# Kernel optimization log

Measured on AMD Instinct MI355X. Metric: run time of the kernel, lower is better.

## Reference

```python
import jax, jax.numpy as jnp
import numpy as np

B, DV, W, H = 64, 2048, 14, 14
DQ, DA, G, DH, NC = 2400, 1200, 2, 1200, 3000


def setup_inputs() -> dict:
    key = jax.random.key(0)
    ks = jax.random.split(key, 14)
    s = lambda k, shp, scale=0.02: jax.random.normal(k, shp, dtype=jnp.float32) * scale
    return {
        "input_q": jax.random.normal(ks[0], (B, DQ), dtype=jnp.float32),
        "input_v": jax.random.normal(ks[1], (B, DV, W, H), dtype=jnp.float32),
        "Wv_att": s(ks[2], (DA, DV)),
        "bv_att": s(ks[3], (DA,)),
        "Wq_att": s(ks[4], (DA, DQ)),
        "bq_att": s(ks[5], (DA,)),
        "Watt": s(ks[6], (G, DA)),
        "batt": s(ks[7], (G,)),
        "Wv_fus": s(ks[8], (G, DH, DV)),
        "bv_fus": s(ks[9], (G, DH)),
        "Wq_fus": s(ks[10], (G * DH, DQ)),
        "bq_fus": s(ks[11], (G * DH,)),
        "Wc": s(ks[12], (NC, G * DH)),
        "bc": s(ks[13], (NC,)),
    }


def reference(input_q, input_v, Wv_att, bv_att, Wq_att, bq_att, Watt, batt,
              Wv_fus, bv_fus, Wq_fus, bq_fus, Wc, bc):
    b, dv, w, h = input_v.shape
    n = w * h  # spatial positions

    # --- attention branch (eval mode: dropout = identity) ---
    # 1x1 conv == per-position linear over channels; activation_v = tanh
    xv = jnp.tanh(jnp.einsum('bchw,dc->bdhw', input_v, Wv_att) + bv_att[None, :, None, None])
    xv = xv.reshape(b, -1, n).transpose(0, 2, 1)               # [B, WH, DA]
    # question projection; activation_q = tanh
    xq = jnp.tanh(input_q @ Wq_att.T + bq_att)                 # [B, DA]
    # MLB Hadamard fusion + activation_mm = tanh
    xatt = jnp.tanh(xv * xq[:, None, :])                       # [B, WH, DA]
    # glimpse scores: 1x1 conv over dim_mm channels
    wgt = jnp.einsum('bnd,gd->bgn', xatt, Watt) + batt[None, :, None]  # [B, G, WH]
    att = jax.nn.softmax(wgt, axis=-1)                         # softmax over WH per glimpse

    # weighted sum of ORIGINAL features per glimpse
    v_flat = input_v.reshape(b, dv, n)                         # [B, DV, WH]
    v_att = jnp.einsum('bgn,bdn->bgd', att, v_flat)            # [B, G, DV]

    # --- glimpse fusion + classification ---
    v_fus = jnp.tanh(jnp.einsum('bgd,ghd->bgh', v_att, Wv_fus) + bv_fus)  # [B, G, DH]
    v_fus = v_fus.reshape(b, -1)                               # [B, G*DH] (concat over glimpses)
    q_fus = jnp.tanh(input_q @ Wq_fus.T + bq_fus)              # [B, G*DH]
    x = (v_fus * q_fus) @ Wc.T + bc                            # [B, NC]
    return (x, wgt)
```

## Files before the change

kernel.cpp:

```cpp
#include <hip/hip_runtime.h>
#include <hip/hip_fp16.h>

typedef _Float16 half8 __attribute__((ext_vector_type(8)));
typedef float f32x4 __attribute__((ext_vector_type(4)));

__device__ __forceinline__ float tanh_fast(float x) {
  float e = __expf(2.0f * x);
  return 1.0f - 2.0f / (e + 1.0f);
}

__device__ __forceinline__ void gload16(const _Float16* g, _Float16* l) {
  __builtin_amdgcn_global_load_lds((const __attribute__((address_space(1))) void*)g,
                                   (__attribute__((address_space(3))) void*)l,
                                   16, 0, 0);
}

__global__ __launch_bounds__(256) void k_transpose_v(const float* __restrict__ in,
                                                     _Float16* __restrict__ out) {
  __shared__ float t[64][65];
  int b = blockIdx.z;
  int c0 = blockIdx.y * 64;
  int p0 = blockIdx.x * 64;
  int tid = threadIdx.x;
  int pl = tid & 63;
  #pragma unroll
  for (int s = 0; s < 16; ++s) {
    int cl = (tid >> 6) + s * 4;
    int p = p0 + pl;
    t[cl][pl] = (p < 196) ? in[((size_t)b * 2048 + (c0 + cl)) * 196 + p] : 0.0f;
  }
  __syncthreads();
  int c8 = (tid & 7) * 8;
  #pragma unroll
  for (int s = 0; s < 2; ++s) {
    int p = p0 + (tid >> 3) + s * 32;
    if (p < 196) {
      half8 v;
      #pragma unroll
      for (int j = 0; j < 8; ++j) v[j] = (_Float16)t[c8 + j][(tid >> 3) + s * 32];
      *(half8*)(out + ((size_t)b * 196 + p) * 2048 + c0 + c8) = v;
    }
  }
}

__global__ __launch_bounds__(256) void k_prep(const float* __restrict__ W,
                                              _Float16* __restrict__ Wh,
                                              const float* __restrict__ batt,
                                              float* __restrict__ wgt) {
  int i = blockIdx.x * 256 + threadIdx.x;
  int n = i >> 11;
  Wh[i] = (n < 1200) ? (_Float16)W[i] : (_Float16)0.0f;
  if (i < 25088) wgt[i] = batt[(i / 196) & 1];
}

__global__ __launch_bounds__(512, 2) void k_gemm1(const _Float16* __restrict__ A,
                                                  const _Float16* __restrict__ B,
                                                  const float* __restrict__ bias,
                                                  const float* __restrict__ xq,
                                                  const float* __restrict__ Watt,
                                                  float* __restrict__ wgt) {
  __shared__ __align__(16) _Float16 AS[2][256 * 64];
  __shared__ __align__(16) _Float16 BS[2][256 * 64];
  int tid = threadIdx.x;
  int n0 = blockIdx.x * 256;
  int m0 = blockIdx.y * 256;
  int lane = tid & 63;
  int wave = tid >> 6;
  int wm = (wave >> 2) * 128;
  int wn = (wave & 3) * 64;
  int fr = lane & 15;
  int fq = lane >> 4;

  int lr = lane >> 3;
  int swz8 = ((lane & 7) ^ lr) << 3;
  const _Float16* aSrc[2][2];
  const _Float16* bSrc[2][2];
  int aDst[2][2], bDst[2][2];
  #pragma unroll
  for (int h = 0; h < 2; ++h)
    #pragma unroll
    for (int j = 0; j < 2; ++j) {
      int ra = j * 128 + h * 64 + wave * 8;
      aSrc[h][j] = A + (size_t)(m0 + ra + lr) * 2048 + swz8;
      aDst[h][j] = ra * 64;
      int rb = (j * 2 + (wave >> 2)) * 64 + h * 32 + (wave & 3) * 8;
      bSrc[h][j] = B + (size_t)(n0 + rb + lr) * 2048 + swz8;
      bDst[h][j] = rb * 64;
    }

  f32x4 acc[8][4];
  #pragma unroll
  for (int i = 0; i < 8; ++i)
    #pragma unroll
    for (int j = 0; j < 4; ++j) acc[i][j] = (f32x4){0.f, 0.f, 0.f, 0.f};

  auto stA = [&](int buf, int h, int k0) {
    gload16(aSrc[h][0] + k0, &AS[buf][aDst[h][0]]);
    gload16(aSrc[h][1] + k0, &AS[buf][aDst[h][1]]);
  };
  auto stB = [&](int buf, int h, int k0) {
    gload16(bSrc[h][0] + k0, &BS[buf][bDst[h][0]]);
    gload16(bSrc[h][1] + k0, &BS[buf][bDst[h][1]]);
  };
  auto dsA = [&](int buf, int mh, half8 (&a)[4][2]) {
    #pragma unroll
    for (int mt = 0; mt < 4; ++mt)
      #pragma unroll
      for (int kk = 0; kk < 2; ++kk) {
        int row = wm + mh * 64 + mt * 16 + fr;
        int c = kk * 4 + fq;
        a[mt][kk] = *(const half8*)(&AS[buf][row * 64 + ((c ^ (row & 7)) << 3)]);
      }
  };
  auto dsB = [&](int buf, int nh, half8 (&b)[2][2]) {
    #pragma unroll
    for (int nt = 0; nt < 2; ++nt)
      #pragma unroll
      for (int kk = 0; kk < 2; ++kk) {
        int row = wn + nh * 32 + nt * 16 + fr;
        int c = kk * 4 + fq;
        b[nt][kk] = *(const half8*)(&BS[buf][row * 64 + ((c ^ (row & 7)) << 3)]);
      }
  };
  auto mma = [&](half8 (&a)[4][2], half8 (&b)[2][2], int mh, int nh) {
    __builtin_amdgcn_s_setprio(1);
    #pragma unroll
    for (int mt = 0; mt < 4; ++mt)
      #pragma unroll
      for (int nt = 0; nt < 2; ++nt)
        #pragma unroll
        for (int kk = 0; kk < 2; ++kk)
          acc[mh * 4 + mt][nh * 2 + nt] = __builtin_amdgcn_mfma_f32_16x16x32_f16(
              a[mt][kk], b[nt][kk], acc[mh * 4 + mt][nh * 2 + nt], 0, 0, 0);
    __builtin_amdgcn_s_setprio(0);
  };

#define BAR() __builtin_amdgcn_s_barrier()
#define LGKM0() do { asm volatile("s_waitcnt lgkmcnt(0)" ::: "memory"); \
                     __builtin_amdgcn_sched_barrier(0); } while (0)

  stA(0, 0, 0); stB(0, 0, 0); stB(0, 1, 0); stA(0, 1, 0);
  stA(1, 0, 64); stB(1, 0, 64); stB(1, 1, 64);
  asm volatile("s_waitcnt vmcnt(6)" ::: "memory");
  BAR();

  half8 a[4][2], b0[2][2], b1[2][2];
  for (int i = 0; i < 16; ++i) {
    const bool nl = (i < 15);
    const int kT = i * 128;
    dsA(0, 0, a); dsB(0, 0, b0);
    stA(1, 1, kT + 64);
    BAR(); LGKM0();
    mma(a, b0, 0, 0);
    BAR();
    dsB(0, 1, b1);
    if (nl) stA(0, 0, kT + 128);
    BAR(); LGKM0();
    mma(a, b1, 0, 1);
    BAR();
    dsA(0, 1, a);
    if (nl) stB(0, 0, kT + 128);
    BAR(); LGKM0();
    mma(a, b1, 1, 1);
    BAR();
    if (nl) {
      stB(0, 1, kT + 128);
      asm volatile("s_waitcnt vmcnt(6)" ::: "memory");
    } else {
      asm volatile("s_waitcnt vmcnt(0)" ::: "memory");
    }
    BAR();
    mma(a, b0, 1, 0);
    BAR();
    dsA(1, 0, a); dsB(1, 0, b0);
    if (nl) stA(0, 1, kT + 128);
    BAR(); LGKM0();
    mma(a, b0, 0, 0);
    BAR();
    dsB(1, 1, b1);
    if (nl) stA(1, 0, kT + 192);
    BAR(); LGKM0();
    mma(a, b1, 0, 1);
    BAR();
    dsA(1, 1, a);
    if (nl) stB(1, 0, kT + 192);
    BAR(); LGKM0();
    mma(a, b1, 1, 1);
    BAR();
    if (nl) {
      stB(1, 1, kT + 192);
      asm volatile("s_waitcnt vmcnt(6)" ::: "memory");
    }
    BAR();
    mma(a, b0, 1, 0);
    BAR();
  }
#undef BAR
#undef LGKM0

  float bcol[4], wa0c[4], wa1c[4], xqv[4];
  int colv[4]; bool okv[4];
  #pragma unroll
  for (int nf = 0; nf < 4; ++nf) {
    int col = n0 + wn + (nf >> 1) * 32 + (nf & 1) * 16 + fr;
    bool ok = col < 1200;
    colv[nf] = col; okv[nf] = ok;
    bcol[nf] = ok ? bias[col] : 0.f;
    wa0c[nf] = ok ? Watt[col] : 0.f;
    wa1c[nf] = ok ? Watt[1200 + col] : 0.f;
    xqv[nf] = 0.f;
  }
  int bprev = -1;
  #pragma unroll
  for (int mf = 0; mf < 8; ++mf) {
    #pragma unroll
    for (int r = 0; r < 4; ++r) {
      int row = m0 + wm + (mf >> 2) * 64 + (mf & 3) * 16 + fq * 4 + r;
      int b = row / 196;
      if (b != bprev) {
        bprev = b;
        #pragma unroll
        for (int nf = 0; nf < 4; ++nf)
          xqv[nf] = okv[nf] ? xq[b * 1200 + colv[nf]] : 0.f;
      }
      float t0 = 0.f, t1 = 0.f;
      #pragma unroll
      for (int nf = 0; nf < 4; ++nf) {
        float xv = tanh_fast(acc[mf][nf][r] + bcol[nf]);
        float xa = tanh_fast(xv * xqv[nf]);
        t0 += xa * wa0c[nf];
        t1 += xa * wa1c[nf];
      }
      #pragma unroll
      for (int off = 8; off > 0; off >>= 1) {
        t0 += __shfl_down(t0, off);
        t1 += __shfl_down(t1, off);
      }
      if (fr == 0) {
        int p = row - b * 196;
        atomicAdd(&wgt[(b * 2 + 0) * 196 + p], t0);
        atomicAdd(&wgt[(b * 2 + 1) * 196 + p], t1);
      }
    }
  }
}

__global__ __launch_bounds__(256) void k_vatt(const _Float16* __restrict__ Vt,
                                              const float* __restrict__ wgt,
                                              float* __restrict__ v_att) {
  __shared__ float a0s[196], a1s[196];
  int b = blockIdx.y;
  int tid = threadIdx.x;
  int wv = tid >> 6, lane = tid & 63;
  if (wv < 2) {
    const float* wr = wgt + ((size_t)b * 2 + wv) * 196;
    float v[4];
    #pragma unroll
    for (int i = 0; i < 4; ++i) {
      int n = lane + i * 64;
      v[i] = (n < 196) ? wr[n] : -1e30f;
    }
    float mx = fmaxf(fmaxf(v[0], v[1]), fmaxf(v[2], v[3]));
    #pragma unroll
    for (int off = 32; off > 0; off >>= 1) mx = fmaxf(mx, __shfl_xor(mx, off));
    float s = 0.f;
    #pragma unroll
    for (int i = 0; i < 4; ++i) {
      int n = lane + i * 64;
      float e = (n < 196) ? __expf(v[i] - mx) : 0.f;
      v[i] = e;
      s += e;
    }
    #pragma unroll
    for (int off = 32; off > 0; off >>= 1) s += __shfl_xor(s, off);
    float inv = 1.f / s;
    float* dst = wv ? a1s : a0s;
    #pragma unroll
    for (int i = 0; i < 4; ++i) {
      int n = lane + i * 64;
      if (n < 196) dst[n] = v[i] * inv;
    }
  }
  __syncthreads();
  int d = blockIdx.x * 256 + tid;
  const _Float16* vp = Vt + (size_t)b * 196 * 2048 + d;
  float s0 = 0.f, s1 = 0.f;
  for (int n = 0; n < 196; ++n) {
    float v = (float)vp[(size_t)n * 2048];
    s0 += a0s[n] * v;
    s1 += a1s[n] * v;
  }
  v_att[((size_t)b * 2 + 0) * 2048 + d] = s0;
  v_att[((size_t)b * 2 + 1) * 2048 + d] = s1;
}

__global__ __launch_bounds__(256) void k_skinnyQ(const float* __restrict__ q,
                                                 const float* __restrict__ Wa,
                                                 const float* __restrict__ Wf,
                                                 int S, float* __restrict__ P) {
  __shared__ __align__(16) float As[32][64];
  __shared__ __align__(16) float Ws2[32][64];
  int tid = threadIdx.x;
  int x = blockIdx.x;
  int s = blockIdx.y;
  bool f = x >= 19;
  const float* W = f ? Wf : Wa;
  int nt0 = f ? (x - 19) * 64 : x * 64;
  int N = f ? 2400 : 1200;
  int colBase = f ? 1200 : 0;
  const int K = 2400;
  int tiles = K >> 5;
  int t0 = (s * tiles) / S;
  int t1 = ((s + 1) * tiles) / S;
  int tx = tid & 15, ty = tid >> 4;
  int lm = tid >> 2;
  int lk = (tid & 3) * 8;
  const float* Ab = q + (size_t)lm * K;
  int ng = nt0 + lm;
  const float* Wb = W + (size_t)ng * K;
  bool wok = ng < N;
  float acc[4][4] = {};
  for (int t = t0; t < t1; ++t) {
    int k0 = t * 32;
    __syncthreads();
    #pragma unroll
    for (int j = 0; j < 8; ++j) As[lk + j][lm] = Ab[k0 + lk + j];
    #pragma unroll
    for (int j = 0; j < 8; ++j) Ws2[lk + j][lm] = wok ? Wb[k0 + lk + j] : 0.0f;
    __syncthreads();
    #pragma unroll
    for (int kk = 0; kk < 32; ++kk) {
      f32x4 a = *(const f32x4*)&As[kk][ty * 4];
      f32x4 wv = *(const f32x4*)&Ws2[kk][tx * 4];
      #pragma unroll
      for (int i = 0; i < 4; ++i)
        #pragma unroll
        for (int j = 0; j < 4; ++j) acc[i][j] += a[i] * wv[j];
    }
  }
  #pragma unroll
  for (int i = 0; i < 4; ++i) {
    int m = ty * 4 + i;
    #pragma unroll
    for (int j = 0; j < 4; ++j) {
      int nl = nt0 + tx * 4 + j;
      if (nl < N) P[((size_t)s * 64 + m) * 3600 + colBase + nl] = acc[i][j];
    }
  }
}

__global__ __launch_bounds__(256) void k_combineQ(const float* __restrict__ P, int S,
                                                  const float* __restrict__ bq_att,
                                                  const float* __restrict__ bq_fus,
                                                  float* __restrict__ xq,
                                                  float* __restrict__ q_fus) {
  int i = blockIdx.x * 256 + threadIdx.x;
  if (i >= 230400) return;
  int row = i / 3600, col = i % 3600;
  float sum = 0.f;
  for (int ss = 0; ss < S; ++ss) sum += P[(size_t)ss * 230400 + i];
  if (col < 1200) xq[row * 1200 + col] = tanh_fast(sum + bq_att[col]);
  else            q_fus[row * 2400 + col - 1200] = tanh_fast(sum + bq_fus[col - 1200]);
}

__global__ __launch_bounds__(256) void k_skinny(const float* __restrict__ A1,
                                                const float* __restrict__ A2,
                                                int lda, int strideAz,
                                                const float* __restrict__ W, long strideWz,
                                                int N, int K, int S,
                                                float* __restrict__ P, int ldp, int colOffZ) {
  __shared__ __align__(16) float As[32][64];
  __shared__ __align__(16) float Ws2[32][64];
  int tid = threadIdx.x;
  int z = blockIdx.z;
  int s = blockIdx.y;
  int nt0 = blockIdx.x * 64;
  int tiles = K >> 5;
  int t0 = (s * tiles) / S;
  int t1 = ((s + 1) * tiles) / S;
  int tx = tid & 15, ty = tid >> 4;
  int lm = tid >> 2;
  int lk = (tid & 3) * 8;
  const float* Ab = A1 + (size_t)z * strideAz + (size_t)lm * lda;
  const float* A2b = A2 ? (A2 + (size_t)z * strideAz + (size_t)lm * lda) : nullptr;
  int ng = nt0 + lm;
  const float* Wb = W + (size_t)z * strideWz + (size_t)ng * K;
  bool wok = ng < N;
  float acc[4][4] = {};
  for (int t = t0; t < t1; ++t) {
    int k0 = t * 32;
    __syncthreads();
    #pragma unroll
    for (int j = 0; j < 8; ++j) {
      float v = Ab[k0 + lk + j];
      if (A2b) v *= A2b[k0 + lk + j];
      As[lk + j][lm] = v;
    }
    #pragma unroll
    for (int j = 0; j < 8; ++j) Ws2[lk + j][lm] = wok ? Wb[k0 + lk + j] : 0.0f;
    __syncthreads();
    #pragma unroll
    for (int kk = 0; kk < 32; ++kk) {
      f32x4 a = *(const f32x4*)&As[kk][ty * 4];
      f32x4 wv = *(const f32x4*)&Ws2[kk][tx * 4];
      #pragma unroll
      for (int i = 0; i < 4; ++i)
        #pragma unroll
        for (int j = 0; j < 4; ++j) acc[i][j] += a[i] * wv[j];
    }
  }
  #pragma unroll
  for (int i = 0; i < 4; ++i) {
    int m = ty * 4 + i;
    #pragma unroll
    for (int j = 0; j < 4; ++j) {
      int nl = nt0 + tx * 4 + j;
      if (nl < N) P[((size_t)s * 64 + m) * ldp + z * colOffZ + nl] = acc[i][j];
    }
  }
}

__global__ __launch_bounds__(256) void k_combineVh(const float* __restrict__ P, int S,
                                                   const float* __restrict__ bv_fus,
                                                   const float* __restrict__ q_fus,
                                                   float* __restrict__ h) {
  int i = blockIdx.x * 256 + threadIdx.x;
  if (i >= 153600) return;
  int col = i % 2400;
  float sum = bv_fus[col];
  for (int ss = 0; ss < S; ++ss) sum += P[(size_t)ss * 153600 + i];
  h[i] = tanh_fast(sum) * q_fus[i];
}

__global__ __launch_bounds__(256) void k_combine(const float* __restrict__ P, int S, int ldp,
                                                 const float* __restrict__ bias,
                                                 float* __restrict__ out, int total) {
  int i = blockIdx.x * 256 + threadIdx.x;
  if (i >= total) return;
  float sum = bias[i % ldp];
  for (int ss = 0; ss < S; ++ss) sum += P[(size_t)ss * total + i];
  out[i] = sum;
}

extern "C" void kernel_launch(void* const* d_in, const int* in_sizes, int n_in,
                              void* d_out, int out_size, void* d_ws, size_t ws_size,
                              hipStream_t stream) {
  const float* input_q = (const float*)d_in[0];
  const float* input_v = (const float*)d_in[1];
  const float* Wv_att  = (const float*)d_in[2];
  const float* bv_att  = (const float*)d_in[3];
  const float* Wq_att  = (const float*)d_in[4];
  const float* bq_att  = (const float*)d_in[5];
  const float* Watt    = (const float*)d_in[6];
  const float* batt    = (const float*)d_in[7];
  const float* Wv_fus  = (const float*)d_in[8];
  const float* bv_fus  = (const float*)d_in[9];
  const float* Wq_fus  = (const float*)d_in[10];
  const float* bq_fus  = (const float*)d_in[11];
  const float* Wc      = (const float*)d_in[12];
  const float* bc      = (const float*)d_in[13];
  float* out = (float*)d_out;

  char* ws = (char*)d_ws;
  _Float16* Vt   = (_Float16*)ws; ws += 51380224;
  _Float16* Wh   = (_Float16*)ws; ws += 5242880;
  float* xq      = (float*)ws;    ws += 307200;
  float* v_att   = (float*)ws;    ws += 1048576;
  float* v_fus   = (float*)ws;    ws += 614400;
  float* q_fus   = (float*)ws;    ws += 614400;
  float* P       = (float*)ws;    ws += 14745600;

  float* x_out   = out;
  float* wgt_out = out + 192000;

  const int S = 16;

  k_transpose_v<<<dim3(4, 32, 64), dim3(256), 0, stream>>>(input_v, Vt);
  k_prep<<<dim3(10240), dim3(256), 0, stream>>>(Wv_att, Wh, batt, wgt_out);

  k_skinnyQ<<<dim3(57, S), dim3(256), 0, stream>>>(input_q, Wq_att, Wq_fus, S, P);
  k_combineQ<<<dim3(900), dim3(256), 0, stream>>>(P, S, bq_att, bq_fus, xq, q_fus);

  k_gemm1<<<dim3(5, 49), dim3(512), 0, stream>>>(Vt, Wh, bv_att, xq, Watt, wgt_out);

  k_vatt<<<dim3(8, 64), dim3(256), 0, stream>>>(Vt, wgt_out, v_att);

  k_skinny<<<dim3(19, S, 2), dim3(256), 0, stream>>>(v_att, nullptr, 4096, 2048,
                                                     Wv_fus, 1200L * 2048L, 1200, 2048, S, P, 2400, 1200);
  k_combineVh<<<dim3(600), dim3(256), 0, stream>>>(P, S, bv_fus, q_fus, v_fus);

  k_skinny<<<dim3(47, S, 1), dim3(256), 0, stream>>>(v_fus, nullptr, 2400, 0,
                                                     Wc, 0, 3000, 2400, S, P, 3000, 0);
  k_combine<<<dim3(750), dim3(256), 0, stream>>>(P, S, 3000, bc, x_out, 192000);
}
```

Baseline: 443.2 us.

## Remap GEMM tiles per XCD, relax LDS waits, vectorize attention-weighted sum

The main GEMM now remaps its linear block index so that consecutive tile indices land on the same XCD, which is meant to improve L2 reuse of the shared A and B panels. It also replaces the sched_barrier-based LDS waits with partial lgkmcnt waits and compiler fences, letting the scheduler overlap more work. Separately, the v_att kernel now reads 8 halves per thread and splits the 196 positions across four thread groups, combining the partial sums through shared memory. This cuts per-element load overhead but adds a reduction step and launches fewer blocks.

```diff
diff --git a/kernel.cpp b/kernel.cpp
--- a/kernel.cpp
+++ b/kernel.cpp
@@ -62,8 +62,12 @@
   __shared__ __align__(16) _Float16 AS[2][256 * 64];
   __shared__ __align__(16) _Float16 BS[2][256 * 64];
   int tid = threadIdx.x;
-  int n0 = blockIdx.x * 256;
-  int m0 = blockIdx.y * 256;
+  int lin = blockIdx.y * 5 + blockIdx.x;
+  int xcd = lin & 7;
+  int loc = lin >> 3;
+  int nw = (xcd < 5 ? xcd * 31 : 155 + (xcd - 5) * 30) + loc;
+  int n0 = (nw % 5) * 256;
+  int m0 = (nw / 5) * 256;
   int lane = tid & 63;
   int wave = tid >> 6;
   int wm = (wave >> 2) * 128;
@@ -136,13 +140,15 @@
   };
 
 #define BAR() __builtin_amdgcn_s_barrier()
-#define LGKM0() do { asm volatile("s_waitcnt lgkmcnt(0)" ::: "memory"); \
-                     __builtin_amdgcn_sched_barrier(0); } while (0)
+#define FENCE() asm volatile("" ::: "memory")
+#define LGKM0() asm volatile("s_waitcnt lgkmcnt(0)")
+#define LGKM8() asm volatile("s_waitcnt lgkmcnt(8)")
 
   stA(0, 0, 0); stB(0, 0, 0); stB(0, 1, 0); stA(0, 1, 0);
   stA(1, 0, 64); stB(1, 0, 64); stB(1, 1, 64);
   asm volatile("s_waitcnt vmcnt(6)" ::: "memory");
   BAR();
+  FENCE();
 
   half8 a[4][2], b0[2][2], b1[2][2];
   for (int i = 0; i < 16; ++i) {
@@ -150,6 +156,7 @@
     const int kT = i * 128;
     dsA(0, 0, a); dsB(0, 0, b0);
     stA(1, 1, kT + 64);
+    LGKM8();
     BAR(); LGKM0();
     mma(a, b0, 0, 0);
     BAR();
@@ -170,10 +177,12 @@
       asm volatile("s_waitcnt vmcnt(0)" ::: "memory");
     }
     BAR();
+    FENCE();
     mma(a, b0, 1, 0);
     BAR();
     dsA(1, 0, a); dsB(1, 0, b0);
     if (nl) stA(0, 1, kT + 128);
+    LGKM8();
     BAR(); LGKM0();
     mma(a, b0, 0, 0);
     BAR();
@@ -192,11 +201,14 @@
       asm volatile("s_waitcnt vmcnt(6)" ::: "memory");
     }
     BAR();
+    FENCE();
     mma(a, b0, 1, 0);
     BAR();
   }
 #undef BAR
+#undef FENCE
 #undef LGKM0
+#undef LGKM8
 
   float bcol[4], wa0c[4], wa1c[4], xqv[4];
   int colv[4]; bool okv[4];
@@ -245,10 +257,11 @@
   }
 }
 
-__global__ __launch_bounds__(256) void k_vatt(const _Float16* __restrict__ Vt,
+__global__ __launch_bounds__(512) void k_vatt(const _Float16* __restrict__ Vt,
                                               const float* __restrict__ wgt,
                                               float* __restrict__ v_att) {
   __shared__ float a0s[196], a1s[196];
+  __shared__ float red[2][3][128][9];
   int b = blockIdx.y;
   int tid = threadIdx.x;
   int wv = tid >> 6, lane = tid & 63;
@@ -282,16 +295,43 @@
     }
   }
   __syncthreads();
-  int d = blockIdx.x * 256 + tid;
+  int nc = tid >> 7;
+  int dl = tid & 127;
+  int d = blockIdx.x * 1024 + dl * 8;
   const _Float16* vp = Vt + (size_t)b * 196 * 2048 + d;
-  float s0 = 0.f, s1 = 0.f;
-  for (int n = 0; n < 196; ++n) {
-    float v = (float)vp[(size_t)n * 2048];
-    s0 += a0s[n] * v;
-    s1 += a1s[n] * v;
-  }
-  v_att[((size_t)b * 2 + 0) * 2048 + d] = s0;
-  v_att[((size_t)b * 2 + 1) * 2048 + d] = s1;
+  float s0[8] = {}, s1[8] = {};
+  for (int n = nc * 49; n < nc * 49 + 49; ++n) {
+    half8 v = *(const half8*)(vp + (size_t)n * 2048);
+    float a0 = a0s[n], a1 = a1s[n];
+    #pragma unroll
+    for (int j = 0; j < 8; ++j) {
+      float f = (float)v[j];
+      s0[j] += a0 * f;
+      s1[j] += a1 * f;
+    }
+  }
+  if (nc > 0) {
+    #pragma unroll
+    for (int j = 0; j < 8; ++j) {
+      red[0][nc - 1][dl][j] = s0[j];
+      red[1][nc - 1][dl][j] = s1[j];
+    }
+  }
+  __syncthreads();
+  if (nc == 0) {
+    #pragma unroll
+    for (int c = 0; c < 3; ++c)
+      #pragma unroll
+      for (int j = 0; j < 8; ++j) {
+        s0[j] += red[0][c][dl][j];
+        s1[j] += red[1][c][dl][j];
+      }
+    #pragma unroll
+    for (int j = 0; j < 8; ++j) {
+      v_att[((size_t)b * 2 + 0) * 2048 + d + j] = s0[j];
+      v_att[((size_t)b * 2 + 1) * 2048 + d + j] = s1[j];
+    }
+  }
 }
 
 __global__ __launch_bounds__(256) void k_skinnyQ(const float* __restrict__ q,
@@ -483,7 +523,7 @@
 
   k_gemm1<<<dim3(5, 49), dim3(512), 0, stream>>>(Vt, Wh, bv_att, xq, Watt, wgt_out);
 
-  k_vatt<<<dim3(8, 64), dim3(256), 0, stream>>>(Vt, wgt_out, v_att);
+  k_vatt<<<dim3(2, 64), dim3(512), 0, stream>>>(Vt, wgt_out, v_att);
 
   k_skinny<<<dim3(19, S, 2), dim3(256), 0, stream>>>(v_att, nullptr, 4096, 2048,
                                                      Wv_fus, 1200L * 2048L, 1200, 2048, S, P, 2400, 1200);
```

After: 444.9 us. About the same (+0.4%).
